# Kernel tuning notes

Hardware: AMD Instinct MI355X
Metric: run time of the kernel (lower is better)

## Reference

```python
import jax, jax.numpy as jnp
import numpy as np

MODEL_DIM = 2048
NUM_HEADS = 32
HEAD_DIM = 64
NUM_KV_HEADS = 8
ROPE_BASE = 10000.0
BATCH = 2
SEQ = 2048


def setup_inputs() -> dict:
    key = jax.random.key(0)
    ks = jax.random.split(key, 5)
    sd = 1.0 / np.sqrt(MODEL_DIM)
    x = jax.random.normal(ks[0], (BATCH, SEQ, MODEL_DIM), dtype=jnp.float32)
    Wq = jax.random.normal(ks[1], (MODEL_DIM, NUM_HEADS * HEAD_DIM), dtype=jnp.float32) * sd
    Wk = jax.random.normal(ks[2], (MODEL_DIM, NUM_KV_HEADS * HEAD_DIM), dtype=jnp.float32) * sd
    Wv = jax.random.normal(ks[3], (MODEL_DIM, NUM_KV_HEADS * HEAD_DIM), dtype=jnp.float32) * sd
    Wo = jax.random.normal(ks[4], (NUM_HEADS * HEAD_DIM, MODEL_DIM), dtype=jnp.float32) * sd
    return {"x": x, "Wq": Wq, "Wk": Wk, "Wv": Wv, "Wo": Wo}


def _rope_cache(seq_len, head_dim, base, dtype):
    # inv_freq over even dims, standard rotate-half (Llama-style) RoPE cache
    inv_freq = 1.0 / (base ** (jnp.arange(0, head_dim, 2, dtype=jnp.float32) / head_dim))
    t = jnp.arange(seq_len, dtype=jnp.float32)
    freqs = jnp.outer(t, inv_freq)               # [S, hd/2]
    emb = jnp.concatenate([freqs, freqs], axis=-1)  # [S, hd]
    return jnp.cos(emb).astype(dtype), jnp.sin(emb).astype(dtype)


def _rotate_half(x):
    h = x.shape[-1] // 2
    return jnp.concatenate([-x[..., h:], x[..., :h]], axis=-1)


def _apply_rope(q, k, cos, sin):
    # q,k: [B, H, S, hd]; cos,sin: [S, hd] -> broadcast over batch/heads
    cos = cos[None, None, :, :]
    sin = sin[None, None, :, :]
    q = q * cos + _rotate_half(q) * sin
    k = k * cos + _rotate_half(k) * sin
    return q, k


def reference(x, Wq, Wk, Wv, Wo):
    bsz, seq_len, _ = x.shape
    q_per_kv = NUM_HEADS // NUM_KV_HEADS

    # projections -> [B, H, S, hd]
    q = (x @ Wq).reshape(bsz, seq_len, NUM_HEADS, HEAD_DIM).transpose(0, 2, 1, 3)
    k = (x @ Wk).reshape(bsz, seq_len, NUM_KV_HEADS, HEAD_DIM).transpose(0, 2, 1, 3)
    v = (x @ Wv).reshape(bsz, seq_len, NUM_KV_HEADS, HEAD_DIM).transpose(0, 2, 1, 3)

    # GQA: repeat_interleave KV heads to match Q heads
    k = jnp.repeat(k, q_per_kv, axis=1)
    v = jnp.repeat(v, q_per_kv, axis=1)

    cos, sin = _rope_cache(seq_len, HEAD_DIM, ROPE_BASE, x.dtype)
    q, k = _apply_rope(q, k, cos, sin)

    scale = 1.0 / np.sqrt(HEAD_DIM)
    scores = jnp.einsum('bhqd,bhkd->bhqk', q, k) * scale  # [B,H,S,S]
    causal = jnp.tril(jnp.ones((seq_len, seq_len), dtype=bool))
    scores = jnp.where(causal[None, None], scores, jnp.finfo(scores.dtype).min)
    attn = jax.nn.softmax(scores, axis=-1)
    y = jnp.einsum('bhqk,bhkd->bhqd', attn, v)  # [B,H,S,hd]

    y = y.transpose(0, 2, 1, 3).reshape(bsz, seq_len, NUM_HEADS * HEAD_DIM)
    return y @ Wo
```

## Files before the change

kernel.cpp:

```cpp
#include <hip/hip_runtime.h>
#include <cstdint>

typedef unsigned short u16;
typedef __attribute__((ext_vector_type(8))) short short8;
typedef __attribute__((ext_vector_type(4))) float f32x4;

#define SEQ     2048
#define NHEADS  32
#define NKV     8
#define HD      64
#define DM      2048
#define MROWS   4096
#define KVSTR   1024
#define PSTR    88

__device__ __forceinline__ float b2f(unsigned int u) {
    return __builtin_bit_cast(float, u << 16);
}
__device__ __forceinline__ u16 f2b(float f) {
    unsigned int u = __builtin_bit_cast(unsigned int, f);
    return (u16)((u + 0x7fffu + ((u >> 16) & 1u)) >> 16);
}

#define GLOAD_LDS16(g, l)                                              \
    __builtin_amdgcn_global_load_lds(                                  \
        (const __attribute__((address_space(1))) void*)(g),            \
        (__attribute__((address_space(3))) void*)(l), 16, 0, 0)

__global__ __launch_bounds__(256) void cvt_f32_bf16(
    const float* __restrict__ in, u16* __restrict__ out, int n4) {
    int i = blockIdx.x * 256 + threadIdx.x;
    if (i < n4) {
        float4 v = ((const float4*)in)[i];
        ushort4 o;
        o.x = f2b(v.x); o.y = f2b(v.y); o.z = f2b(v.z); o.w = f2b(v.w);
        ((ushort4*)out)[i] = o;
    }
}

__global__ __launch_bounds__(256) void rope_table_kernel(
    float* __restrict__ cosT, float* __restrict__ sinT) {
    int idx = blockIdx.x * 256 + threadIdx.x;
    int s  = idx >> 5;
    int dl = idx & 31;
    float inv_freq = exp2f((float)dl * -0.41524101186092025f);
    float ang = (float)s * inv_freq;
    float sn, cs;
    sincosf(ang, &sn, &cs);
    cosT[idx] = cs;
    sinT[idx] = sn;
}

__global__ __launch_bounds__(256) void transpose_f32_bf16(
    const float* __restrict__ in, u16* __restrict__ out, int K, int N) {
    __shared__ float tile[32][33];
    int n0 = blockIdx.x * 32, k0 = blockIdx.y * 32;
    int tx = threadIdx.x, ty = threadIdx.y;
    for (int r = ty; r < 32; r += 8)
        tile[r][tx] = in[(size_t)(k0 + r) * N + n0 + tx];
    __syncthreads();
    for (int r = ty; r < 32; r += 8)
        out[(size_t)(n0 + r) * K + k0 + tx] = f2b(tile[tx][r]);
}

#define GEMM_BODY(A, BT, Kdim)                                             \
    constexpr int BK = 32;                                                 \
    __shared__ __align__(16) u16 As[128 * BK];                             \
    __shared__ __align__(16) u16 Bs[128 * BK];                             \
    const int tid  = threadIdx.x;                                          \
    const int wid  = tid >> 6;                                             \
    const int lane = tid & 63;                                             \
    const int quad = lane >> 4;                                            \
    const int l16  = lane & 15;                                            \
    const int rowBase = blockIdx.y * 128;                                  \
    const int colBase = blockIdx.x * 128;                                  \
    const int wr = (wid >> 1) * 64;                                        \
    const int wc = (wid & 1) * 64;                                         \
    const int srow = wid * 32 + (lane >> 2);                               \
    const int scol = (lane & 3) * 8;                                       \
    const u16* gA = (A)  + (size_t)(rowBase + srow) * (Kdim) + scol;       \
    const u16* gB = (BT) + (size_t)(colBase + srow) * (Kdim) + scol;       \
    u16* lA0 = &As[(wid * 32) * BK];                                       \
    u16* lA1 = &As[(wid * 32 + 16) * BK];                                  \
    u16* lB0 = &Bs[(wid * 32) * BK];                                       \
    u16* lB1 = &Bs[(wid * 32 + 16) * BK];                                  \
    const size_t row16 = (size_t)16 * (Kdim);                              \
    f32x4 acc[4][4] = {};                                                  \
    for (int k0 = 0; k0 < (Kdim); k0 += BK) {                              \
        GLOAD_LDS16(gA + k0,         lA0);                                 \
        GLOAD_LDS16(gA + k0 + row16, lA1);                                 \
        GLOAD_LDS16(gB + k0,         lB0);                                 \
        GLOAD_LDS16(gB + k0 + row16, lB1);                                 \
        __syncthreads();                                                   \
        short8 a[4], b[4];                                                 \
        _Pragma("unroll")                                                  \
        for (int mi = 0; mi < 4; ++mi)                                     \
            a[mi] = *(const short8*)&As[(wr + mi * 16 + l16) * BK + quad * 8]; \
        _Pragma("unroll")                                                  \
        for (int ni = 0; ni < 4; ++ni)                                     \
            b[ni] = *(const short8*)&Bs[(wc + ni * 16 + l16) * BK + quad * 8]; \
        _Pragma("unroll")                                                  \
        for (int mi = 0; mi < 4; ++mi)                                     \
            _Pragma("unroll")                                              \
            for (int ni = 0; ni < 4; ++ni)                                 \
                acc[mi][ni] = __builtin_amdgcn_mfma_f32_16x16x32_bf16(     \
                    a[mi], b[ni], acc[mi][ni], 0, 0, 0);                   \
        __syncthreads();                                                   \
    }                                                                      \
    const int wRow = rowBase + wr;                                         \
    const int wCol = colBase + wc;

__global__ __launch_bounds__(256) void gemm_qkv(
    const u16* __restrict__ A, const u16* __restrict__ BT,
    u16* __restrict__ Qb, u16* __restrict__ KVb,
    const float* __restrict__ cosT, const float* __restrict__ sinT) {
    GEMM_BODY(A, BT, DM)

    u16* dst;
    int dstride, dcol;
    float scale;
    bool doRope;
    if (wCol < 2048)      { dst = Qb;  dstride = 2048; dcol = wCol;        scale = 0.125f; doRope = true;  }
    else if (wCol < 2560) { dst = KVb; dstride = 1024; dcol = wCol - 2048; scale = 1.0f;   doRope = true;  }
    else                  { dst = KVb; dstride = 1024; dcol = wCol - 2048; scale = 1.0f;   doRope = false; }

#pragma unroll
    for (int mi = 0; mi < 4; ++mi) {
#pragma unroll
        for (int r = 0; r < 4; ++r) {
            const int R = wRow + mi * 16 + quad * 4 + r;
            u16* crow = dst + (size_t)R * dstride + dcol;
            if (doRope) {
                const int s = R & (SEQ - 1);
#pragma unroll
                for (int ni = 0; ni < 2; ++ni) {
                    const int dl = ni * 16 + l16;
                    float lo = acc[mi][ni][r];
                    float hi = acc[mi][ni + 2][r];
                    float cs = cosT[s * 32 + dl];
                    float sn = sinT[s * 32 + dl];
                    crow[dl]      = f2b((lo * cs - hi * sn) * scale);
                    crow[dl + 32] = f2b((hi * cs + lo * sn) * scale);
                }
            } else {
#pragma unroll
                for (int ni = 0; ni < 4; ++ni)
                    crow[ni * 16 + l16] = f2b(acc[mi][ni][r]);
            }
        }
    }
}

__global__ __launch_bounds__(256) void gemm_out(
    const u16* __restrict__ A, const u16* __restrict__ BT,
    float* __restrict__ C32) {
    GEMM_BODY(A, BT, DM)
#pragma unroll
    for (int mi = 0; mi < 4; ++mi) {
#pragma unroll
        for (int r = 0; r < 4; ++r) {
            const int R = wRow + mi * 16 + quad * 4 + r;
            float* crow = C32 + (size_t)R * DM + wCol;
#pragma unroll
            for (int ni = 0; ni < 4; ++ni)
                crow[ni * 16 + l16] = acc[mi][ni][r];
        }
    }
}

__global__ __launch_bounds__(256) void flash_attn(
    const u16* __restrict__ Q, const u16* __restrict__ KV,
    u16* __restrict__ Y) {
    __shared__ __align__(16) u16 Ks[64 * 64];
    __shared__ __align__(16) u16 Vt[64 * 72];
    __shared__ __align__(16) u16 Ps[4 * 32 * PSTR];

    const int h   = blockIdx.y;
    const int b   = blockIdx.z;
    const int kvh = h >> 2;
    const int tid  = threadIdx.x;
    const int wid  = tid >> 6;
    const int lane = tid & 63;
    const int quad = lane >> 4;
    const int l16  = lane & 15;

    const u16* Kg = KV + (size_t)b * SEQ * KVSTR + kvh * HD;
    const u16* Vg = Kg + 512;
    u16* Psw = Ps + wid * 32 * PSTR;

    const int kc0 = tid,        kKey0 = kc0 >> 3, kCc0 = kc0 & 7;
    const int kc1 = 256 + tid,  kKey1 = kc1 >> 3, kCc1 = kc1 & 7;
    const int vkp = tid & 31;
    const int vd0 = (tid >> 5) * 8;

    for (int half = 0; half < 2; ++half) {
        const int qt = half ? (15 - blockIdx.x) : blockIdx.x;
        const int rowBaseW = qt * 128 + wid * 32;

        short8 qf[2][2];
#pragma unroll
        for (int mt = 0; mt < 2; ++mt)
#pragma unroll
            for (int ks = 0; ks < 2; ++ks)
                qf[mt][ks] = *(const short8*)&Q[
                    (size_t)(b * SEQ + rowBaseW + mt * 16 + l16) * (NHEADS * HD)
                    + h * HD + ks * 32 + quad * 8];

        f32x4 o[2][4] = {};
        float mi[2][4], li[2][4];
#pragma unroll
        for (int mt = 0; mt < 2; ++mt)
#pragma unroll
            for (int r = 0; r < 4; ++r) { mi[mt][r] = -3e38f; li[mt][r] = 0.f; }

        const int nTiles = 2 * qt + 2;

        short8 kreg0 = *(const short8*)&Kg[(size_t)kKey0 * KVSTR + kCc0 * 8];
        short8 kreg1 = *(const short8*)&Kg[(size_t)kKey1 * KVSTR + kCc1 * 8];
        short8 vrA   = *(const short8*)&Vg[(size_t)(2 * vkp)     * KVSTR + vd0];
        short8 vrB   = *(const short8*)&Vg[(size_t)(2 * vkp + 1) * KVSTR + vd0];

        for (int t = 0; t < nTiles; ++t) {
            const int j0 = t * 64;
            __syncthreads();

            *(short8*)&Ks[kKey0 * 64 + ((kCc0 ^ (kKey0 & 7)) * 8)] = kreg0;
            *(short8*)&Ks[kKey1 * 64 + ((kCc1 ^ (kKey1 & 7)) * 8)] = kreg1;
#pragma unroll
            for (int i = 0; i < 8; ++i) {
                unsigned int w = (unsigned int)(u16)vrA[i]
                               | ((unsigned int)(u16)vrB[i] << 16);
                ((unsigned int*)Vt)[(vd0 + i) * 36 + vkp] = w;
            }
            __syncthreads();

            if (t + 1 < nTiles) {
                const size_t jn = (size_t)(j0 + 64);
                kreg0 = *(const short8*)&Kg[(jn + kKey0) * KVSTR + kCc0 * 8];
                kreg1 = *(const short8*)&Kg[(jn + kKey1) * KVSTR + kCc1 * 8];
                vrA   = *(const short8*)&Vg[(jn + 2 * vkp)     * KVSTR + vd0];
                vrB   = *(const short8*)&Vg[(jn + 2 * vkp + 1) * KVSTR + vd0];
            }

            f32x4 s[2][4] = {};
#pragma unroll
            for (int ks = 0; ks < 2; ++ks)
#pragma unroll
                for (int ct = 0; ct < 4; ++ct) {
                    int key = ct * 16 + l16;
                    int cc  = (ks * 4 + quad) ^ (key & 7);
                    short8 bk = *(const short8*)&Ks[key * 64 + cc * 8];
#pragma unroll
                    for (int mt = 0; mt < 2; ++mt)
                        s[mt][ct] = __builtin_amdgcn_mfma_f32_16x16x32_bf16(
                            qf[mt][ks], bk, s[mt][ct], 0, 0, 0);
                }

            if (j0 + 63 > rowBaseW) {
#pragma unroll
                for (int mt = 0; mt < 2; ++mt)
#pragma unroll
                    for (int ct = 0; ct < 4; ++ct)
#pragma unroll
                        for (int r = 0; r < 4; ++r) {
                            int R = rowBaseW + mt * 16 + quad * 4 + r;
                            int J = j0 + ct * 16 + l16;
                            if (J > R) s[mt][ct][r] = -3e38f;
                        }
            }

#pragma unroll
            for (int mt = 0; mt < 2; ++mt)
#pragma unroll
                for (int r = 0; r < 4; ++r) {
                    float rmax = fmaxf(fmaxf(s[mt][0][r], s[mt][1][r]),
                                       fmaxf(s[mt][2][r], s[mt][3][r]));
                    rmax = fmaxf(rmax, __shfl_xor(rmax, 1, 64));
                    rmax = fmaxf(rmax, __shfl_xor(rmax, 2, 64));
                    rmax = fmaxf(rmax, __shfl_xor(rmax, 4, 64));
                    rmax = fmaxf(rmax, __shfl_xor(rmax, 8, 64));
                    float mnew  = fmaxf(mi[mt][r], rmax);
                    float alpha = __expf(mi[mt][r] - mnew);
                    mi[mt][r] = mnew;
                    float rs = 0.f;
#pragma unroll
                    for (int ct = 0; ct < 4; ++ct) {
                        float p = __expf(s[mt][ct][r] - mnew);
                        s[mt][ct][r] = p;
                        rs += p;
                        o[mt][ct][r] *= alpha;
                    }
                    rs += __shfl_xor(rs, 1, 64);
                    rs += __shfl_xor(rs, 2, 64);
                    rs += __shfl_xor(rs, 4, 64);
                    rs += __shfl_xor(rs, 8, 64);
                    li[mt][r] = li[mt][r] * alpha + rs;
                }

#pragma unroll
            for (int mt = 0; mt < 2; ++mt)
#pragma unroll
                for (int ct = 0; ct < 4; ++ct)
#pragma unroll
                    for (int r = 0; r < 4; ++r)
                        Psw[(mt * 16 + quad * 4 + r) * PSTR + ct * 16 + l16] =
                            f2b(s[mt][ct][r]);

            short8 pa[2][2];
#pragma unroll
            for (int mt = 0; mt < 2; ++mt)
#pragma unroll
                for (int ks = 0; ks < 2; ++ks)
                    pa[mt][ks] = *(const short8*)&Psw[(mt * 16 + l16) * PSTR + ks * 32 + quad * 8];
#pragma unroll
            for (int ks = 0; ks < 2; ++ks)
#pragma unroll
                for (int ct = 0; ct < 4; ++ct) {
                    short8 vbf = *(const short8*)&Vt[(ct * 16 + l16) * 72 + ks * 32 + quad * 8];
#pragma unroll
                    for (int mt = 0; mt < 2; ++mt)
                        o[mt][ct] = __builtin_amdgcn_mfma_f32_16x16x32_bf16(
                            pa[mt][ks], vbf, o[mt][ct], 0, 0, 0);
                }
        }

#pragma unroll
        for (int mt = 0; mt < 2; ++mt) {
            float rli[4];
#pragma unroll
            for (int r = 0; r < 4; ++r) rli[r] = 1.0f / li[mt][r];
#pragma unroll
            for (int r = 0; r < 4; ++r) {
                int R = rowBaseW + mt * 16 + quad * 4 + r;
                u16* yrow = Y + (size_t)(b * SEQ + R) * (NHEADS * HD) + h * HD;
#pragma unroll
                for (int ct = 0; ct < 4; ++ct)
                    yrow[ct * 16 + l16] = f2b(o[mt][ct][r] * rli[r]);
            }
        }
    }
}

extern "C" void kernel_launch(void* const* d_in, const int* in_sizes, int n_in,
                              void* d_out, int out_size, void* d_ws, size_t ws_size,
                              hipStream_t stream) {
    const float* x  = (const float*)d_in[0];
    const float* Wq = (const float*)d_in[1];
    const float* Wk = (const float*)d_in[2];
    const float* Wv = (const float*)d_in[3];
    const float* Wo = (const float*)d_in[4];
    float* out = (float*)d_out;

    char* ws = (char*)d_ws;
    u16*  xb    = (u16*)(ws);
    u16*  WqkvT = (u16*)(ws + 16777216);
    u16*  WoT   = (u16*)(ws + 29360128);
    u16*  Qb    = (u16*)(ws + 37748736);
    u16*  KVb   = (u16*)(ws + 54525952);
    u16*  Yb    = (u16*)(ws + 62914560);
    float* cosT = (float*)(ws + 79691776);
    float* sinT = (float*)(ws + 79953920);

    rope_table_kernel<<<dim3(65536 / 256), 256, 0, stream>>>(cosT, sinT);

    cvt_f32_bf16<<<dim3(MROWS * DM / 4 / 256), 256, 0, stream>>>(x, xb, MROWS * DM / 4);

    dim3 tb(32, 8);
    transpose_f32_bf16<<<dim3(2048/32, 2048/32), tb, 0, stream>>>(Wq, WqkvT, 2048, 2048);
    transpose_f32_bf16<<<dim3( 512/32, 2048/32), tb, 0, stream>>>(Wk, WqkvT + 2048 * 2048, 2048, 512);
    transpose_f32_bf16<<<dim3( 512/32, 2048/32), tb, 0, stream>>>(Wv, WqkvT + 2560 * 2048, 2048, 512);
    transpose_f32_bf16<<<dim3(2048/32, 2048/32), tb, 0, stream>>>(Wo, WoT, 2048, 2048);

    gemm_qkv<<<dim3(24, 32), 256, 0, stream>>>(xb, WqkvT, Qb, KVb, cosT, sinT);

    flash_attn<<<dim3(8, NHEADS, 2), 256, 0, stream>>>(Qb, KVb, Yb);

    gemm_out<<<dim3(16, 32), 256, 0, stream>>>(Yb, WoT, out);
}
```

Before: 400.7 us.

## Split flash attention work across 8 waves with 16 query rows each

The flash attention block grows from 256 to 512 threads, so each wave handles 16 query rows instead of 32. K/V tile loads into LDS are spread across twice as many threads, and per-wave register state (Q fragments, accumulators, softmax stats) is halved. The aim is more waves in flight for latency hiding and lower register pressure. In exchange, each wave reuses every K/V fragment read from LDS for only one MFMA row tile, which doubles LDS read traffic per FLOP.

```diff
diff --git a/kernel.cpp b/kernel.cpp
--- a/kernel.cpp
+++ b/kernel.cpp
@@ -3,6 +3,7 @@
 
 typedef unsigned short u16;
 typedef __attribute__((ext_vector_type(8))) short short8;
+typedef __attribute__((ext_vector_type(4))) short short4v;
 typedef __attribute__((ext_vector_type(4))) float f32x4;
 
 #define SEQ     2048
@@ -168,12 +169,12 @@
     }
 }
 
-__global__ __launch_bounds__(256) void flash_attn(
+__global__ __launch_bounds__(512, 4) void flash_attn(
     const u16* __restrict__ Q, const u16* __restrict__ KV,
     u16* __restrict__ Y) {
     __shared__ __align__(16) u16 Ks[64 * 64];
     __shared__ __align__(16) u16 Vt[64 * 72];
-    __shared__ __align__(16) u16 Ps[4 * 32 * PSTR];
+    __shared__ __align__(16) u16 Ps[8 * 16 * PSTR];
 
     const int h   = blockIdx.y;
     const int b   = blockIdx.z;
@@ -186,48 +187,41 @@
 
     const u16* Kg = KV + (size_t)b * SEQ * KVSTR + kvh * HD;
     const u16* Vg = Kg + 512;
-    u16* Psw = Ps + wid * 32 * PSTR;
-
-    const int kc0 = tid,        kKey0 = kc0 >> 3, kCc0 = kc0 & 7;
-    const int kc1 = 256 + tid,  kKey1 = kc1 >> 3, kCc1 = kc1 & 7;
-    const int vkp = tid & 31;
-    const int vd0 = (tid >> 5) * 8;
+    u16* Psw = Ps + wid * 16 * PSTR;
+
+    const int kKey = tid >> 3, kCc = tid & 7;
+    const int vkp  = tid & 31;
+    const int vd0  = (tid >> 5) * 4;
 
     for (int half = 0; half < 2; ++half) {
         const int qt = half ? (15 - blockIdx.x) : blockIdx.x;
-        const int rowBaseW = qt * 128 + wid * 32;
-
-        short8 qf[2][2];
-#pragma unroll
-        for (int mt = 0; mt < 2; ++mt)
-#pragma unroll
-            for (int ks = 0; ks < 2; ++ks)
-                qf[mt][ks] = *(const short8*)&Q[
-                    (size_t)(b * SEQ + rowBaseW + mt * 16 + l16) * (NHEADS * HD)
-                    + h * HD + ks * 32 + quad * 8];
-
-        f32x4 o[2][4] = {};
-        float mi[2][4], li[2][4];
-#pragma unroll
-        for (int mt = 0; mt < 2; ++mt)
-#pragma unroll
-            for (int r = 0; r < 4; ++r) { mi[mt][r] = -3e38f; li[mt][r] = 0.f; }
+        const int rowBaseW = qt * 128 + wid * 16;
+
+        short8 qf[2];
+#pragma unroll
+        for (int ks = 0; ks < 2; ++ks)
+            qf[ks] = *(const short8*)&Q[
+                (size_t)(b * SEQ + rowBaseW + l16) * (NHEADS * HD)
+                + h * HD + ks * 32 + quad * 8];
+
+        f32x4 o[4] = {};
+        float mi[4], li[4];
+#pragma unroll
+        for (int r = 0; r < 4; ++r) { mi[r] = -3e38f; li[r] = 0.f; }
 
         const int nTiles = 2 * qt + 2;
 
-        short8 kreg0 = *(const short8*)&Kg[(size_t)kKey0 * KVSTR + kCc0 * 8];
-        short8 kreg1 = *(const short8*)&Kg[(size_t)kKey1 * KVSTR + kCc1 * 8];
-        short8 vrA   = *(const short8*)&Vg[(size_t)(2 * vkp)     * KVSTR + vd0];
-        short8 vrB   = *(const short8*)&Vg[(size_t)(2 * vkp + 1) * KVSTR + vd0];
+        short8  kreg = *(const short8*)&Kg[(size_t)kKey * KVSTR + kCc * 8];
+        short4v vrA  = *(const short4v*)&Vg[(size_t)(2 * vkp)     * KVSTR + vd0];
+        short4v vrB  = *(const short4v*)&Vg[(size_t)(2 * vkp + 1) * KVSTR + vd0];
 
         for (int t = 0; t < nTiles; ++t) {
             const int j0 = t * 64;
             __syncthreads();
 
-            *(short8*)&Ks[kKey0 * 64 + ((kCc0 ^ (kKey0 & 7)) * 8)] = kreg0;
-            *(short8*)&Ks[kKey1 * 64 + ((kCc1 ^ (kKey1 & 7)) * 8)] = kreg1;
-#pragma unroll
-            for (int i = 0; i < 8; ++i) {
+            *(short8*)&Ks[kKey * 64 + ((kCc ^ (kKey & 7)) * 8)] = kreg;
+#pragma unroll
+            for (int i = 0; i < 4; ++i) {
                 unsigned int w = (unsigned int)(u16)vrA[i]
                                | ((unsigned int)(u16)vrB[i] << 16);
                 ((unsigned int*)Vt)[(vd0 + i) * 36 + vkp] = w;
@@ -236,13 +230,12 @@
 
             if (t + 1 < nTiles) {
                 const size_t jn = (size_t)(j0 + 64);
-                kreg0 = *(const short8*)&Kg[(jn + kKey0) * KVSTR + kCc0 * 8];
-                kreg1 = *(const short8*)&Kg[(jn + kKey1) * KVSTR + kCc1 * 8];
-                vrA   = *(const short8*)&Vg[(jn + 2 * vkp)     * KVSTR + vd0];
-                vrB   = *(const short8*)&Vg[(jn + 2 * vkp + 1) * KVSTR + vd0];
-            }
-
-            f32x4 s[2][4] = {};
+                kreg = *(const short8*)&Kg[(jn + kKey) * KVSTR + kCc * 8];
+                vrA  = *(const short4v*)&Vg[(jn + 2 * vkp)     * KVSTR + vd0];
+                vrB  = *(const short4v*)&Vg[(jn + 2 * vkp + 1) * KVSTR + vd0];
+            }
+
+            f32x4 s[4] = {};
 #pragma unroll
             for (int ks = 0; ks < 2; ++ks)
 #pragma unroll
@@ -250,93 +243,77 @@
                     int key = ct * 16 + l16;
                     int cc  = (ks * 4 + quad) ^ (key & 7);
                     short8 bk = *(const short8*)&Ks[key * 64 + cc * 8];
-#pragma unroll
-                    for (int mt = 0; mt < 2; ++mt)
-                        s[mt][ct] = __builtin_amdgcn_mfma_f32_16x16x32_bf16(
-                            qf[mt][ks], bk, s[mt][ct], 0, 0, 0);
+                    s[ct] = __builtin_amdgcn_mfma_f32_16x16x32_bf16(
+                        qf[ks], bk, s[ct], 0, 0, 0);
                 }
 
             if (j0 + 63 > rowBaseW) {
 #pragma unroll
-                for (int mt = 0; mt < 2; ++mt)
-#pragma unroll
-                    for (int ct = 0; ct < 4; ++ct)
-#pragma unroll
-                        for (int r = 0; r < 4; ++r) {
-                            int R = rowBaseW + mt * 16 + quad * 4 + r;
-                            int J = j0 + ct * 16 + l16;
-                            if (J > R) s[mt][ct][r] = -3e38f;
-                        }
-            }
-
-#pragma unroll
-            for (int mt = 0; mt < 2; ++mt)
-#pragma unroll
-                for (int r = 0; r < 4; ++r) {
-                    float rmax = fmaxf(fmaxf(s[mt][0][r], s[mt][1][r]),
-                                       fmaxf(s[mt][2][r], s[mt][3][r]));
-                    rmax = fmaxf(rmax, __shfl_xor(rmax, 1, 64));
-                    rmax = fmaxf(rmax, __shfl_xor(rmax, 2, 64));
-                    rmax = fmaxf(rmax, __shfl_xor(rmax, 4, 64));
-                    rmax = fmaxf(rmax, __shfl_xor(rmax, 8, 64));
-                    float mnew  = fmaxf(mi[mt][r], rmax);
-                    float alpha = __expf(mi[mt][r] - mnew);
-                    mi[mt][r] = mnew;
-                    float rs = 0.f;
-#pragma unroll
-                    for (int ct = 0; ct < 4; ++ct) {
-                        float p = __expf(s[mt][ct][r] - mnew);
-                        s[mt][ct][r] = p;
-                        rs += p;
-                        o[mt][ct][r] *= alpha;
+                for (int ct = 0; ct < 4; ++ct)
+#pragma unroll
+                    for (int r = 0; r < 4; ++r) {
+                        int R = rowBaseW + quad * 4 + r;
+                        int J = j0 + ct * 16 + l16;
+                        if (J > R) s[ct][r] = -3e38f;
                     }
-                    rs += __shfl_xor(rs, 1, 64);
-                    rs += __shfl_xor(rs, 2, 64);
-                    rs += __shfl_xor(rs, 4, 64);
-                    rs += __shfl_xor(rs, 8, 64);
-                    li[mt][r] = li[mt][r] * alpha + rs;
+            }
+
+#pragma unroll
+            for (int r = 0; r < 4; ++r) {
+                float rmax = fmaxf(fmaxf(s[0][r], s[1][r]),
+                                   fmaxf(s[2][r], s[3][r]));
+                rmax = fmaxf(rmax, __shfl_xor(rmax, 1, 64));
+                rmax = fmaxf(rmax, __shfl_xor(rmax, 2, 64));
+                rmax = fmaxf(rmax, __shfl_xor(rmax, 4, 64));
+                rmax = fmaxf(rmax, __shfl_xor(rmax, 8, 64));
+                float mnew  = fmaxf(mi[r], rmax);
+                float alpha = __expf(mi[r] - mnew);
+                mi[r] = mnew;
+                float rs = 0.f;
+#pragma unroll
+                for (int ct = 0; ct < 4; ++ct) {
+                    float p = __expf(s[ct][r] - mnew);
+                    s[ct][r] = p;
+                    rs += p;
+                    o[ct][r] *= alpha;
                 }
-
-#pragma unroll
-            for (int mt = 0; mt < 2; ++mt)
-#pragma unroll
-                for (int ct = 0; ct < 4; ++ct)
-#pragma unroll
-                    for (int r = 0; r < 4; ++r)
-                        Psw[(mt * 16 + quad * 4 + r) * PSTR + ct * 16 + l16] =
-                            f2b(s[mt][ct][r]);
-
-            short8 pa[2][2];
-#pragma unroll
-            for (int mt = 0; mt < 2; ++mt)
-#pragma unroll
-                for (int ks = 0; ks < 2; ++ks)
-                    pa[mt][ks] = *(const short8*)&Psw[(mt * 16 + l16) * PSTR + ks * 32 + quad * 8];
+                rs += __shfl_xor(rs, 1, 64);
+                rs += __shfl_xor(rs, 2, 64);
+                rs += __shfl_xor(rs, 4, 64);
+                rs += __shfl_xor(rs, 8, 64);
+                li[r] = li[r] * alpha + rs;
+            }
+
+#pragma unroll
+            for (int ct = 0; ct < 4; ++ct)
+#pragma unroll
+                for (int r = 0; r < 4; ++r)
+                    Psw[(quad * 4 + r) * PSTR + ct * 16 + l16] = f2b(s[ct][r]);
+
+            short8 pa[2];
+#pragma unroll
+            for (int ks = 0; ks < 2; ++ks)
+                pa[ks] = *(const short8*)&Psw[l16 * PSTR + ks * 32 + quad * 8];
 #pragma unroll
             for (int ks = 0; ks < 2; ++ks)
 #pragma unroll
                 for (int ct = 0; ct < 4; ++ct) {
                     short8 vbf = *(const short8*)&Vt[(ct * 16 + l16) * 72 + ks * 32 + quad * 8];
-#pragma unroll
-                    for (int mt = 0; mt < 2; ++mt)
-                        o[mt][ct] = __builtin_amdgcn_mfma_f32_16x16x32_bf16(
-                            pa[mt][ks], vbf, o[mt][ct], 0, 0, 0);
+                    o[ct] = __builtin_amdgcn_mfma_f32_16x16x32_bf16(
+                        pa[ks], vbf, o[ct], 0, 0, 0);
                 }
         }
 
-#pragma unroll
-        for (int mt = 0; mt < 2; ++mt) {
-            float rli[4];
-#pragma unroll
-            for (int r = 0; r < 4; ++r) rli[r] = 1.0f / li[mt][r];
-#pragma unroll
-            for (int r = 0; r < 4; ++r) {
-                int R = rowBaseW + mt * 16 + quad * 4 + r;
-                u16* yrow = Y + (size_t)(b * SEQ + R) * (NHEADS * HD) + h * HD;
-#pragma unroll
-                for (int ct = 0; ct < 4; ++ct)
-                    yrow[ct * 16 + l16] = f2b(o[mt][ct][r] * rli[r]);
-            }
+        float rli[4];
+#pragma unroll
+        for (int r = 0; r < 4; ++r) rli[r] = 1.0f / li[r];
+#pragma unroll
+        for (int r = 0; r < 4; ++r) {
+            int R = rowBaseW + quad * 4 + r;
+            u16* yrow = Y + (size_t)(b * SEQ + R) * (NHEADS * HD) + h * HD;
+#pragma unroll
+            for (int ct = 0; ct < 4; ++ct)
+                yrow[ct * 16 + l16] = f2b(o[ct][r] * rli[r]);
         }
     }
 }
@@ -373,7 +350,7 @@
 
     gemm_qkv<<<dim3(24, 32), 256, 0, stream>>>(xb, WqkvT, Qb, KVb, cosT, sinT);
 
-    flash_attn<<<dim3(8, NHEADS, 2), 256, 0, stream>>>(Qb, KVb, Yb);
+    flash_attn<<<dim3(8, NHEADS, 2), 512, 0, stream>>>(Qb, KVb, Yb);
 
     gemm_out<<<dim3(16, 32), 256, 0, stream>>>(Yb, WoT, out);
 }
```

Result: faster. 390.5 us (-2.5%).
